# Kernel optimization log

Hardware: AMD Instinct MI355X
Metric: run time of the kernel (lower is better)

The kernel has to match this reference:

```python
import jax, jax.numpy as jnp
import numpy as np

HEAD = 12
EPS = float(np.finfo(np.float32).eps)  # torch RMSNorm default eps = finfo(dtype).eps


def _rmsnorm(v, g):
    # v: [B,H,T,dh], g: [dh]
    ms = jnp.mean(v * v, axis=-1, keepdims=True)
    return v * jax.lax.rsqrt(ms + EPS) * g


def setup_inputs() -> dict:
    key = jax.random.key(0)
    k1, k2, k3, k4, k5 = jax.random.split(key, 5)
    B, T, C = 2, 2048, 768
    x = jax.random.normal(k1, (B, T, C), dtype=jnp.float32)
    # nn.Linear(feats, feats, bias=False) weight: [out, in]
    W = jax.random.normal(k2, (C, C), dtype=jnp.float32) * (1.0 / np.sqrt(C))
    dh = C // HEAD
    g1 = jnp.ones((dh,), dtype=jnp.float32)
    g2 = jnp.ones((dh,), dtype=jnp.float32)
    g3 = jnp.ones((dh,), dtype=jnp.float32)
    return {"x": x, "W": W, "g1": g1, "g2": g2, "g3": g3}


def reference(x, W, g1, g2, g3):
    B, T, C = x.shape
    dh = C // HEAD
    sqrt_d = np.sqrt(dh).astype(np.float32)
    # qkv projection (shared weights): w = x @ W.T -> [B,H,T,dh]
    w = (x @ W.T).reshape(B, T, HEAD, dh).transpose(0, 2, 1, 3)
    q = _rmsnorm(w, g1)
    k = _rmsnorm(w, g2)
    v = _rmsnorm(w, g3)
    # full T x T score matrix (intentionally materialized, as in the module)
    att = jnp.einsum('bhif,bhjf->bhij', q, k) / sqrt_d
    a = jax.nn.softmax(att, axis=-1) + jax.nn.softmax(att, axis=-2)  # bisoftmax
    y = jnp.einsum('bhij,bhjf->bihf', a, v).reshape(B, T, C)
    # F.linear(y, W.t()) == y @ W
    return y @ W
```

## Files before the change

kernel.cpp:

```cpp
#include <hip/hip_runtime.h>

constexpr int T_SEQ = 2048;
constexpr int CDIM  = 768;
constexpr int HEADS = 12;
constexpr int DH    = 64;
constexpr int BATCH = 2;
constexpr int BH_TOT = BATCH * HEADS;
constexpr int NROWS  = BATCH * T_SEQ;
constexpr float RMS_EPS = 1.1920929e-07f;
constexpr float QSCALE = 0.18033688011112042f;

typedef __attribute__((ext_vector_type(8))) short bf16x8;
typedef __attribute__((ext_vector_type(4))) float f32x4;
typedef __attribute__((ext_vector_type(4))) unsigned int u32x4;

__device__ __forceinline__ unsigned short f2bf(float f) {
    union { float f; unsigned int u; } v; v.f = f;
    unsigned int u = v.u;
    unsigned int r = (u + 0x7fffu + ((u >> 16) & 1u)) >> 16;
    return (unsigned short)r;
}
__device__ __forceinline__ float b2f(unsigned short h) {
    union { unsigned int u; float f; } v; v.u = ((unsigned int)h) << 16;
    return v.f;
}
__device__ __forceinline__ unsigned int cvt_pk_bf16(float lo, float hi) {
    unsigned int r;
    asm("v_cvt_pk_bf16_f32 %0, %1, %2" : "=v"(r) : "v"(lo), "v"(hi));
    return r;
}
__device__ __forceinline__ float fast_exp2(float x) {
    float r;
    asm("v_exp_f32 %0, %1" : "=v"(r) : "v"(x));
    return r;
}
__device__ __forceinline__ void gld_lds16(const void* g, void* l) {
    __builtin_amdgcn_global_load_lds(
        (const __attribute__((address_space(1))) void*)g,
        (__attribute__((address_space(3))) void*)l, 16, 0, 0);
}
__device__ __forceinline__ void stage16k(const unsigned short* gbase, unsigned short* lbase, int tid) {
#pragma unroll
    for (int p = 0; p < 4; ++p) {
        int d = (p * 256 + tid) * 16;
        int gb = d ^ (((d >> 7) & 7) << 4);
        gld_lds16((const char*)gbase + gb, (char*)lbase + d);
    }
}
__device__ __forceinline__ void stageV16k(const unsigned short* vbase, int jbyte0,
                                          unsigned short* lbase, int tid) {
#pragma unroll
    for (int p = 0; p < 4; ++p) {
        int d = (p * 256 + tid) * 16;
        int f = d >> 8;
        int cb = (d & 255) ^ ((f & 7) << 4);
        gld_lds16((const char*)vbase + (size_t)f * (T_SEQ * 2) + jbyte0 + cb,
                  (char*)lbase + d);
    }
}

__global__ __launch_bounds__(256) void prep_kernel(
    const float* __restrict__ x, const float* __restrict__ W,
    unsigned short* __restrict__ xh,
    unsigned short* __restrict__ Wh, unsigned short* __restrict__ WTh)
{
    const size_t NC = (size_t)NROWS * CDIM;
    const size_t WSZ = (size_t)CDIM * CDIM;
    size_t stride = (size_t)gridDim.x * blockDim.x;
    for (size_t i = (size_t)blockIdx.x * blockDim.x + threadIdx.x; i < NC; i += stride)
        xh[i] = f2bf(x[i]);
    for (size_t i = (size_t)blockIdx.x * blockDim.x + threadIdx.x; i < WSZ; i += stride) {
        unsigned short h = f2bf(W[i]);
        Wh[i] = h;
        size_t k = i / CDIM, c = i % CDIM;
        WTh[c * CDIM + k] = h;
    }
}

__global__ __launch_bounds__(256) void gemm64_nt(
    const unsigned short* __restrict__ A, const unsigned short* __restrict__ B,
    float* __restrict__ C, int M, int N, int K, int ldc)
{
    __shared__ unsigned short sA[64 * 64], sB[64 * 64];
    const int tid = threadIdx.x;
    const int lane = tid & 63;
    const int wv = tid >> 6;
    const int wr = wv >> 1, wc = wv & 1;
    const int li = lane & 15, g = lane >> 4;
    const int M0 = blockIdx.y * 64, N0 = blockIdx.x * 64;

    f32x4 acc[2][2];
#pragma unroll
    for (int i = 0; i < 2; ++i)
#pragma unroll
        for (int j = 0; j < 2; ++j) acc[i][j] = (f32x4)0.0f;

    for (int k0 = 0; k0 < K; k0 += 64) {
        __syncthreads();
#pragma unroll
        for (int p = 0; p < 2; ++p) {
            int dd = tid * 16 + p * 4096;
            int row = dd >> 7;
            int cb = (dd & 127) ^ ((row & 7) << 4);
            gld_lds16((const char*)A + ((size_t)(M0 + row) * K + k0) * 2 + cb, (char*)sA + dd);
            gld_lds16((const char*)B + ((size_t)(N0 + row) * K + k0) * 2 + cb, (char*)sB + dd);
        }
        __syncthreads();
#pragma unroll
        for (int ks = 0; ks < 2; ++ks) {
            const int ko = ks * 32 + g * 8;
            bf16x8 a[2], b[2];
#pragma unroll
            for (int mi = 0; mi < 2; ++mi) {
                int r = wr * 32 + mi * 16 + li;
                a[mi] = *(const bf16x8*)((char*)sA + ((r * 128 + ko * 2) ^ ((r & 7) << 4)));
            }
#pragma unroll
            for (int ni = 0; ni < 2; ++ni) {
                int r = wc * 32 + ni * 16 + li;
                b[ni] = *(const bf16x8*)((char*)sB + ((r * 128 + ko * 2) ^ ((r & 7) << 4)));
            }
#pragma unroll
            for (int mi = 0; mi < 2; ++mi)
#pragma unroll
                for (int ni = 0; ni < 2; ++ni)
                    acc[mi][ni] = __builtin_amdgcn_mfma_f32_16x16x32_bf16(a[mi], b[ni], acc[mi][ni], 0, 0, 0);
        }
    }
#pragma unroll
    for (int mi = 0; mi < 2; ++mi)
#pragma unroll
        for (int ni = 0; ni < 2; ++ni)
#pragma unroll
            for (int r = 0; r < 4; ++r) {
                int row = M0 + wr * 32 + mi * 16 + g * 4 + r;
                int col = N0 + wc * 32 + ni * 16 + li;
                C[(size_t)row * ldc + col] = acc[mi][ni][r];
            }
}

__global__ __launch_bounds__(256) void rmsqkv_kernel(
    const float* __restrict__ wbuf,
    const float* __restrict__ g1, const float* __restrict__ g2, const float* __restrict__ g3,
    unsigned short* __restrict__ qb, unsigned short* __restrict__ kb,
    unsigned short* __restrict__ vb)
{
    const int lane = threadIdx.x & 63;
    const int wv = threadIdx.x >> 6;
    const int ridx = blockIdx.x * 4 + wv;
    const int bt = ridx / HEADS;
    const int h = ridx % HEADS;
    const int b = bt >> 11, t = bt & (T_SEQ - 1);

    float v = wbuf[(size_t)bt * CDIM + h * DH + lane];
    float ss = v * v;
#pragma unroll
    for (int m = 32; m; m >>= 1) ss += __shfl_xor(ss, m);
    float r = rsqrtf(ss * (1.0f / 64.0f) + RMS_EPS);
    float wn = v * r;

    size_t o = ((size_t)(b * HEADS + h) * T_SEQ + t) * DH + lane;
    qb[o] = f2bf(wn * g1[lane] * QSCALE);
    kb[o] = f2bf(wn * g2[lane]);
    vb[o] = f2bf(wn * g3[lane]);
}

__global__ __launch_bounds__(256) void vtrans_kernel(
    const unsigned short* __restrict__ vb, unsigned short* __restrict__ vT)
{
    __shared__ unsigned short tile[64][65];
    const int bh = blockIdx.y, t0 = blockIdx.x * 64;
    const int tid = threadIdx.x;
    const int c = tid & 63, r4 = tid >> 6;
#pragma unroll
    for (int i = 0; i < 16; ++i) {
        int rr = r4 + i * 4;
        tile[rr][c] = vb[((size_t)bh * T_SEQ + t0 + rr) * DH + c];
    }
    __syncthreads();
#pragma unroll
    for (int i = 0; i < 16; ++i) {
        int ff = r4 + i * 4;
        vT[((size_t)bh * DH + ff) * T_SEQ + t0 + c] = tile[c][ff];
    }
}

__global__ __launch_bounds__(256) void sums_kernel(
    const unsigned short* __restrict__ qb, const unsigned short* __restrict__ kb,
    float* __restrict__ rowsum, float* __restrict__ colsum)
{
    __shared__ unsigned short sQ[2][128 * 64];
    const int tid = threadIdx.x;
    const int lane = tid & 63;
    const int w = tid >> 6;
    const int li = lane & 15;
    const int g = lane >> 4;
    const int bh = blockIdx.z;
    const int J0 = blockIdx.x * 128;
    const int IC = blockIdx.y * 512;

    bf16x8 kf[2][2];
#pragma unroll
    for (int jb = 0; jb < 2; ++jb)
#pragma unroll
        for (int ks = 0; ks < 2; ++ks)
            kf[jb][ks] = *(const bf16x8*)&kb[((size_t)bh * T_SEQ + J0 + w * 32 + jb * 16 + li) * DH
                                            + ks * 32 + g * 8];

    stage16k(&qb[((size_t)bh * T_SEQ + IC) * DH], sQ[0], tid);
    __syncthreads();

    float csum[2][4];
#pragma unroll
    for (int jb = 0; jb < 2; ++jb)
#pragma unroll
        for (int r = 0; r < 4; ++r) csum[jb][r] = 0.0f;

    for (int it = 0; it < 4; ++it) {
        const int I0 = IC + it * 128;
        if (it + 1 < 4)
            stage16k(&qb[((size_t)bh * T_SEQ + I0 + 128) * DH], sQ[(it + 1) & 1], tid);
        const unsigned short* q = sQ[it & 1];

#pragma unroll
        for (int half = 0; half < 2; ++half) {
            f32x4 acc[2][4];
#pragma unroll
            for (int jb = 0; jb < 2; ++jb)
#pragma unroll
                for (int ib = 0; ib < 4; ++ib) acc[jb][ib] = (f32x4)0.0f;
#pragma unroll
            for (int ks = 0; ks < 2; ++ks) {
                const int ko = ks * 32 + g * 8;
#pragma unroll
                for (int ib = 0; ib < 4; ++ib) {
                    int qr = half * 64 + ib * 16 + li;
                    bf16x8 qf = *(const bf16x8*)((const char*)q + ((qr * 128 + ko * 2) ^ ((qr & 7) << 4)));
#pragma unroll
                    for (int jb = 0; jb < 2; ++jb)
                        acc[jb][ib] = __builtin_amdgcn_mfma_f32_16x16x32_bf16(kf[jb][ks], qf, acc[jb][ib], 0, 0, 0);
                }
            }
#pragma unroll
            for (int ib = 0; ib < 4; ++ib) {
                float rp = 0.0f;
#pragma unroll
                for (int jb = 0; jb < 2; ++jb)
#pragma unroll
                    for (int r = 0; r < 4; ++r) {
                        float e = fast_exp2(acc[jb][ib][r]);
                        csum[jb][r] += e;
                        rp += e;
                    }
                rp += __shfl_xor(rp, 16);
                rp += __shfl_xor(rp, 32);
                if (g == 0)
                    atomicAdd(&rowsum[(size_t)bh * T_SEQ + I0 + half * 64 + ib * 16 + li], rp);
            }
        }
        __syncthreads();
    }
#pragma unroll
    for (int jb = 0; jb < 2; ++jb)
#pragma unroll
        for (int r = 0; r < 4; ++r) {
            float c = csum[jb][r];
            c += __shfl_xor(c, 1); c += __shfl_xor(c, 2);
            c += __shfl_xor(c, 4); c += __shfl_xor(c, 8);
            if (li == 0)
                atomicAdd(&colsum[(size_t)bh * T_SEQ + J0 + w * 32 + jb * 16 + g * 4 + r], c);
        }
}

__global__ __launch_bounds__(256) void inv_kernel(
    const float* __restrict__ rs, const float* __restrict__ cs,
    float* __restrict__ ri, float* __restrict__ ci_, int n)
{
    int i = blockIdx.x * 256 + threadIdx.x;
    if (i < n) { ri[i] = 1.0f / rs[i]; ci_[i] = 1.0f / cs[i]; }
}

__global__ __launch_bounds__(256) void fused_pv_kernel(
    const unsigned short* __restrict__ qb, const unsigned short* __restrict__ kb,
    const unsigned short* __restrict__ vT,
    const float* __restrict__ rowinv, const float* __restrict__ colinv,
    float* __restrict__ ypart, int jlen, int nt)
{
    __shared__ unsigned short sK[2][128 * 64];
    __shared__ unsigned short sV[2][64 * 128];
    __shared__ unsigned short sP[64 * 128];

    const int tid = threadIdx.x;
    const int lane = tid & 63;
    const int w = tid >> 6;
    const int li = lane & 15;
    const int g = lane >> 4;
    const int bh = blockIdx.z;
    const int jc = blockIdx.y;
    const int I0 = blockIdx.x * 64;
    const int J0 = jc * jlen;

    const int qrow = I0 + w * 16 + li;
    bf16x8 qf[2];
#pragma unroll
    for (int ks = 0; ks < 2; ++ks)
        qf[ks] = *(const bf16x8*)&qb[((size_t)bh * T_SEQ + qrow) * DH + ks * 32 + g * 8];
    const float rv = rowinv[bh * T_SEQ + qrow];

    const int prow = w * 16 + li;
    const int pkey = (prow & 7) << 4;

    f32x4 accy[4];
#pragma unroll
    for (int i = 0; i < 4; ++i) accy[i] = (f32x4)0.0f;

    const unsigned short* kt0 = &kb[((size_t)bh * T_SEQ + J0) * DH];
    const unsigned short* vb0 = &vT[(size_t)bh * DH * T_SEQ];

    stage16k(kt0, sK[0], tid);
    stageV16k(vb0, J0 * 2, sV[0], tid);

    int buf = 0;
    for (int jt = 0; jt < nt; ++jt) {
        __syncthreads();
        if (jt + 1 < nt) {
            stage16k(kt0 + (size_t)(jt + 1) * 128 * DH, sK[buf ^ 1], tid);
            stageV16k(vb0, (J0 + (jt + 1) * 128) * 2, sV[buf ^ 1], tid);
        }

        f32x4 accs[8];
#pragma unroll
        for (int jb = 0; jb < 8; ++jb) accs[jb] = (f32x4)0.0f;
#pragma unroll
        for (int ks = 0; ks < 2; ++ks) {
            const int ko = ks * 32 + g * 8;
#pragma unroll
            for (int jb = 0; jb < 8; ++jb) {
                int jr = jb * 16 + li;
                bf16x8 kfr = *(const bf16x8*)((char*)sK[buf] + ((jr * 128 + ko * 2) ^ ((jr & 7) << 4)));
                accs[jb] = __builtin_amdgcn_mfma_f32_16x16x32_bf16(kfr, qf[ks], accs[jb], 0, 0, 0);
            }
        }

#pragma unroll
        for (int jb = 0; jb < 8; ++jb) {
            f32x4 cv = *(const f32x4*)&colinv[(size_t)bh * T_SEQ + J0 + jt * 128 + jb * 16 + g * 4];
            float p0 = fast_exp2(accs[jb][0]) * (rv + cv[0]);
            float p1 = fast_exp2(accs[jb][1]) * (rv + cv[1]);
            float p2 = fast_exp2(accs[jb][2]) * (rv + cv[2]);
            float p3 = fast_exp2(accs[jb][3]) * (rv + cv[3]);
            uint2 pw;
            pw.x = cvt_pk_bf16(p0, p1);
            pw.y = cvt_pk_bf16(p2, p3);
            int off = (prow * 256 + jb * 32 + g * 8) ^ pkey;
            *(uint2*)((char*)sP + off) = pw;
        }

#pragma unroll
        for (int ks2 = 0; ks2 < 4; ++ks2) {
            bf16x8 pf = *(const bf16x8*)((char*)sP + ((prow * 256 + ks2 * 64 + g * 16) ^ pkey));
#pragma unroll
            for (int ni = 0; ni < 4; ++ni) {
                int vrow = ni * 16 + li;
                bf16x8 vf = *(const bf16x8*)((char*)sV[buf] + ((vrow * 256 + ks2 * 64 + g * 16) ^ ((vrow & 7) << 4)));
                accy[ni] = __builtin_amdgcn_mfma_f32_16x16x32_bf16(pf, vf, accy[ni], 0, 0, 0);
            }
        }
        buf ^= 1;
    }

#pragma unroll
    for (int ni = 0; ni < 4; ++ni)
#pragma unroll
        for (int r = 0; r < 4; ++r) {
            int i = I0 + w * 16 + g * 4 + r;
            int f = ni * 16 + li;
            ypart[(((size_t)jc * BH_TOT + bh) * T_SEQ + i) * DH + f] = accy[ni][r];
        }
}

__global__ __launch_bounds__(256) void reduce_kernel(
    const float* __restrict__ ypart, unsigned short* __restrict__ yh, int js)
{
    const size_t STR = (size_t)BH_TOT * T_SEQ * DH;
    size_t idx = (size_t)blockIdx.x * 256 + threadIdx.x;
    if (idx >= STR / 4) return;
    f32x4 a = *(const f32x4*)&ypart[idx * 4];
    for (int c = 1; c < js; ++c) {
        f32x4 b = *(const f32x4*)&ypart[(size_t)c * STR + idx * 4];
        a[0] += b[0]; a[1] += b[1]; a[2] += b[2]; a[3] += b[3];
    }
    int e = (int)(idx * 4);
    int f = e & 63;
    int rrow = e >> 6;
    int t = rrow & (T_SEQ - 1);
    int bh = rrow >> 11;
    int b_ = bh / HEADS, h = bh % HEADS;
    size_t o = ((size_t)b_ * T_SEQ + t) * CDIM + h * DH + f;
#pragma unroll
    for (int q = 0; q < 4; ++q)
        yh[o + q] = f2bf(a[q]);
}

extern "C" void kernel_launch(void* const* d_in, const int* in_sizes, int n_in,
                              void* d_out, int out_size, void* d_ws, size_t ws_size,
                              hipStream_t stream)
{
    const float* x  = (const float*)d_in[0];
    const float* W  = (const float*)d_in[1];
    const float* g1 = (const float*)d_in[2];
    const float* g2 = (const float*)d_in[3];
    const float* g3 = (const float*)d_in[4];
    float* out = (float*)d_out;

    char* p = (char*)d_ws;
    auto alloc = [&](size_t bytes) -> void* {
        void* r = (void*)p;
        p += (bytes + 255) & ~(size_t)255;
        return r;
    };
    const size_t NC  = (size_t)NROWS * CDIM;
    const size_t WSZ = (size_t)CDIM * CDIM;
    const size_t QSZ = (size_t)BH_TOT * T_SEQ * DH;

    unsigned short* xh   = (unsigned short*)alloc(NC * 2);
    unsigned short* Wh   = (unsigned short*)alloc(WSZ * 2);
    unsigned short* WTh  = (unsigned short*)alloc(WSZ * 2);
    float*          wbuf = (float*)alloc(NC * 4);
    unsigned short* qb   = (unsigned short*)alloc(QSZ * 2);
    unsigned short* kb   = (unsigned short*)alloc(QSZ * 2);
    unsigned short* vb   = (unsigned short*)alloc(QSZ * 2);
    unsigned short* vT   = (unsigned short*)alloc(QSZ * 2);
    unsigned short* yh   = (unsigned short*)alloc(NC * 2);
    float* rowsum = (float*)alloc((size_t)BH_TOT * T_SEQ * 4);
    float* colsum = (float*)alloc((size_t)BH_TOT * T_SEQ * 4);
    float* rowinv = (float*)alloc((size_t)BH_TOT * T_SEQ * 4);
    float* colinv = (float*)alloc((size_t)BH_TOT * T_SEQ * 4);

    size_t used = (size_t)(p - (char*)d_ws);
    int js = (ws_size >= used + 4 * QSZ * sizeof(float) + (1u << 20)) ? 4 : 2;
    float* ypart = (float*)alloc((size_t)js * QSZ * 4);

    prep_kernel<<<2048, 256, 0, stream>>>(x, W, xh, Wh, WTh);
    gemm64_nt<<<dim3(CDIM / 64, NROWS / 64), 256, 0, stream>>>(
        xh, Wh, wbuf, NROWS, CDIM, CDIM, CDIM);
    rmsqkv_kernel<<<(NROWS * HEADS) / 4, 256, 0, stream>>>(
        wbuf, g1, g2, g3, qb, kb, vb);
    vtrans_kernel<<<dim3(T_SEQ / 64, BH_TOT), 256, 0, stream>>>(vb, vT);

    hipMemsetAsync(rowsum, 0, (size_t)BH_TOT * T_SEQ * 4, stream);
    hipMemsetAsync(colsum, 0, (size_t)BH_TOT * T_SEQ * 4, stream);
    sums_kernel<<<dim3(T_SEQ / 128, 4, BH_TOT), 256, 0, stream>>>(
        qb, kb, rowsum, colsum);
    int n = BH_TOT * T_SEQ;
    inv_kernel<<<(n + 255) / 256, 256, 0, stream>>>(rowsum, colsum, rowinv, colinv, n);

    fused_pv_kernel<<<dim3(T_SEQ / 64, js, BH_TOT), 256, 0, stream>>>(
        qb, kb, vT, rowinv, colinv, ypart, T_SEQ / js, T_SEQ / js / 128);
    {
        size_t n4 = (size_t)BH_TOT * T_SEQ * DH / 4;
        reduce_kernel<<<(unsigned)((n4 + 255) / 256), 256, 0, stream>>>(ypart, yh, js);
    }

    gemm64_nt<<<dim3(CDIM / 64, NROWS / 64), 256, 0, stream>>>(
        yh, WTh, out, NROWS, CDIM, CDIM, CDIM);
}
```

Baseline: 164.4 us.

## Pre-arrange LDS tiles in MFMA fragment order and fix split-J to two

Replaces the XOR-swizzled row-major LDS staging of Q, K, V and the P scratch with layouts stored directly in MFMA fragment order. Each lane's 16-byte fragment read becomes a simple linear offset, which removes swizzle arithmetic and is meant to avoid bank conflicts. The J-split is also hardcoded to two chunks, so the loop trip count is a compile-time constant and the reduce step is a fixed two-way add. The cost is less parallelism in the fused PV kernel than when four splits were chosen, and global loads during staging are now gathered in smaller strided pieces.

```diff
diff --git a/kernel.cpp b/kernel.cpp
--- a/kernel.cpp
+++ b/kernel.cpp
@@ -7,6 +7,7 @@
 constexpr int BATCH = 2;
 constexpr int BH_TOT = BATCH * HEADS;
 constexpr int NROWS  = BATCH * T_SEQ;
+constexpr int JS     = 2;
 constexpr float RMS_EPS = 1.1920929e-07f;
 constexpr float QSCALE = 0.18033688011112042f;
 
@@ -39,23 +40,34 @@
         (const __attribute__((address_space(1))) void*)g,
         (__attribute__((address_space(3))) void*)l, 16, 0, 0);
 }
-__device__ __forceinline__ void stage16k(const unsigned short* gbase, unsigned short* lbase, int tid) {
+__device__ __forceinline__ void stageK(const unsigned short* gbase, unsigned short* lbase, int tid) {
 #pragma unroll
     for (int p = 0; p < 4; ++p) {
-        int d = (p * 256 + tid) * 16;
-        int gb = d ^ (((d >> 7) & 7) << 4);
-        gld_lds16((const char*)gbase + gb, (char*)lbase + d);
-    }
-}
-__device__ __forceinline__ void stageV16k(const unsigned short* vbase, int jbyte0,
-                                          unsigned short* lbase, int tid) {
+        int d16 = p * 256 + tid;
+        int li = d16 & 15, g = (d16 >> 4) & 3, ks = (d16 >> 6) & 1, jb = d16 >> 7;
+        int src = (jb * 16 + li) * 128 + ks * 64 + g * 16;
+        gld_lds16((const char*)gbase + src, (char*)lbase + d16 * 16);
+    }
+}
+__device__ __forceinline__ void stageV(const unsigned short* vbase, int jbyte0,
+                                       unsigned short* lbase, int tid) {
 #pragma unroll
     for (int p = 0; p < 4; ++p) {
-        int d = (p * 256 + tid) * 16;
-        int f = d >> 8;
-        int cb = (d & 255) ^ ((f & 7) << 4);
-        gld_lds16((const char*)vbase + (size_t)f * (T_SEQ * 2) + jbyte0 + cb,
-                  (char*)lbase + d);
+        int d16 = p * 256 + tid;
+        int li = d16 & 15, g = (d16 >> 4) & 3, ni = (d16 >> 6) & 3, ks2 = d16 >> 8;
+        int f = ni * 16 + li;
+        gld_lds16((const char*)vbase + (size_t)f * (T_SEQ * 2) + jbyte0 + ks2 * 64 + g * 16,
+                  (char*)lbase + d16 * 16);
+    }
+}
+__device__ __forceinline__ void stageQ(const unsigned short* gbase, unsigned short* lbase, int tid) {
+#pragma unroll
+    for (int p = 0; p < 4; ++p) {
+        int d16 = p * 256 + tid;
+        int li = d16 & 15, g = (d16 >> 4) & 3, ks = (d16 >> 6) & 1;
+        int ib = (d16 >> 7) & 3, half = (d16 >> 9) & 1;
+        int src = (half * 64 + ib * 16 + li) * 128 + ks * 64 + g * 16;
+        gld_lds16((const char*)gbase + src, (char*)lbase + d16 * 16);
     }
 }
 
@@ -207,7 +219,7 @@
             kf[jb][ks] = *(const bf16x8*)&kb[((size_t)bh * T_SEQ + J0 + w * 32 + jb * 16 + li) * DH
                                             + ks * 32 + g * 8];
 
-    stage16k(&qb[((size_t)bh * T_SEQ + IC) * DH], sQ[0], tid);
+    stageQ(&qb[((size_t)bh * T_SEQ + IC) * DH], sQ[0], tid);
     __syncthreads();
 
     float csum[2][4];
@@ -219,7 +231,7 @@
     for (int it = 0; it < 4; ++it) {
         const int I0 = IC + it * 128;
         if (it + 1 < 4)
-            stage16k(&qb[((size_t)bh * T_SEQ + I0 + 128) * DH], sQ[(it + 1) & 1], tid);
+            stageQ(&qb[((size_t)bh * T_SEQ + I0 + 128) * DH], sQ[(it + 1) & 1], tid);
         const unsigned short* q = sQ[it & 1];
 
 #pragma unroll
@@ -231,11 +243,10 @@
                 for (int ib = 0; ib < 4; ++ib) acc[jb][ib] = (f32x4)0.0f;
 #pragma unroll
             for (int ks = 0; ks < 2; ++ks) {
-                const int ko = ks * 32 + g * 8;
 #pragma unroll
                 for (int ib = 0; ib < 4; ++ib) {
-                    int qr = half * 64 + ib * 16 + li;
-                    bf16x8 qf = *(const bf16x8*)((const char*)q + ((qr * 128 + ko * 2) ^ ((qr & 7) << 4)));
+                    bf16x8 qf = *(const bf16x8*)((const char*)q +
+                        ((((half * 4 + ib) * 2 + ks) * 64 + g * 16 + li) * 16));
 #pragma unroll
                     for (int jb = 0; jb < 2; ++jb)
                         acc[jb][ib] = __builtin_amdgcn_mfma_f32_16x16x32_bf16(kf[jb][ks], qf, acc[jb][ib], 0, 0, 0);
@@ -284,7 +295,7 @@
     const unsigned short* __restrict__ qb, const unsigned short* __restrict__ kb,
     const unsigned short* __restrict__ vT,
     const float* __restrict__ rowinv, const float* __restrict__ colinv,
-    float* __restrict__ ypart, int jlen, int nt)
+    float* __restrict__ ypart)
 {
     __shared__ unsigned short sK[2][128 * 64];
     __shared__ unsigned short sV[2][64 * 128];
@@ -298,7 +309,8 @@
     const int bh = blockIdx.z;
     const int jc = blockIdx.y;
     const int I0 = blockIdx.x * 64;
-    const int J0 = jc * jlen;
+    const int J0 = jc * (T_SEQ / JS);
+    constexpr int NT = T_SEQ / JS / 128;
 
     const int qrow = I0 + w * 16 + li;
     bf16x8 qf[2];
@@ -307,8 +319,7 @@
         qf[ks] = *(const bf16x8*)&qb[((size_t)bh * T_SEQ + qrow) * DH + ks * 32 + g * 8];
     const float rv = rowinv[bh * T_SEQ + qrow];
 
-    const int prow = w * 16 + li;
-    const int pkey = (prow & 7) << 4;
+    char* const sPw = (char*)sP + w * 4096;
 
     f32x4 accy[4];
 #pragma unroll
@@ -317,15 +328,15 @@
     const unsigned short* kt0 = &kb[((size_t)bh * T_SEQ + J0) * DH];
     const unsigned short* vb0 = &vT[(size_t)bh * DH * T_SEQ];
 
-    stage16k(kt0, sK[0], tid);
-    stageV16k(vb0, J0 * 2, sV[0], tid);
+    stageK(kt0, sK[0], tid);
+    stageV(vb0, J0 * 2, sV[0], tid);
 
     int buf = 0;
-    for (int jt = 0; jt < nt; ++jt) {
+    for (int jt = 0; jt < NT; ++jt) {
         __syncthreads();
-        if (jt + 1 < nt) {
-            stage16k(kt0 + (size_t)(jt + 1) * 128 * DH, sK[buf ^ 1], tid);
-            stageV16k(vb0, (J0 + (jt + 1) * 128) * 2, sV[buf ^ 1], tid);
+        if (jt + 1 < NT) {
+            stageK(kt0 + (size_t)(jt + 1) * 128 * DH, sK[buf ^ 1], tid);
+            stageV(vb0, (J0 + (jt + 1) * 128) * 2, sV[buf ^ 1], tid);
         }
 
         f32x4 accs[8];
@@ -333,11 +344,10 @@
         for (int jb = 0; jb < 8; ++jb) accs[jb] = (f32x4)0.0f;
 #pragma unroll
         for (int ks = 0; ks < 2; ++ks) {
-            const int ko = ks * 32 + g * 8;
 #pragma unroll
             for (int jb = 0; jb < 8; ++jb) {
-                int jr = jb * 16 + li;
-                bf16x8 kfr = *(const bf16x8*)((char*)sK[buf] + ((jr * 128 + ko * 2) ^ ((jr & 7) << 4)));
+                bf16x8 kfr = *(const bf16x8*)((char*)sK[buf] +
+                    (((jb * 2 + ks) * 64 + g * 16 + li) * 16));
                 accs[jb] = __builtin_amdgcn_mfma_f32_16x16x32_bf16(kfr, qf[ks], accs[jb], 0, 0, 0);
             }
         }
@@ -352,17 +362,17 @@
             uint2 pw;
             pw.x = cvt_pk_bf16(p0, p1);
             pw.y = cvt_pk_bf16(p2, p3);
-            int off = (prow * 256 + jb * 32 + g * 8) ^ pkey;
-            *(uint2*)((char*)sP + off) = pw;
+            int off = ((jb >> 1) * 4 + (jb & 1) * 2 + (g >> 1)) * 256 + li * 16 + (g & 1) * 8;
+            *(uint2*)(sPw + off) = pw;
         }
 
 #pragma unroll
         for (int ks2 = 0; ks2 < 4; ++ks2) {
-            bf16x8 pf = *(const bf16x8*)((char*)sP + ((prow * 256 + ks2 * 64 + g * 16) ^ pkey));
+            bf16x8 pf = *(const bf16x8*)(sPw + ((ks2 * 4 + g) * 256 + li * 16));
 #pragma unroll
             for (int ni = 0; ni < 4; ++ni) {
-                int vrow = ni * 16 + li;
-                bf16x8 vf = *(const bf16x8*)((char*)sV[buf] + ((vrow * 256 + ks2 * 64 + g * 16) ^ ((vrow & 7) << 4)));
+                bf16x8 vf = *(const bf16x8*)((char*)sV[buf] +
+                    ((ks2 * 256 + ni * 64 + g * 16 + li) * 16));
                 accy[ni] = __builtin_amdgcn_mfma_f32_16x16x32_bf16(pf, vf, accy[ni], 0, 0, 0);
             }
         }
@@ -380,16 +390,13 @@
 }
 
 __global__ __launch_bounds__(256) void reduce_kernel(
-    const float* __restrict__ ypart, unsigned short* __restrict__ yh, int js)
+    const float* __restrict__ ypart, unsigned short* __restrict__ yh)
 {
     const size_t STR = (size_t)BH_TOT * T_SEQ * DH;
     size_t idx = (size_t)blockIdx.x * 256 + threadIdx.x;
     if (idx >= STR / 4) return;
     f32x4 a = *(const f32x4*)&ypart[idx * 4];
-    for (int c = 1; c < js; ++c) {
-        f32x4 b = *(const f32x4*)&ypart[(size_t)c * STR + idx * 4];
-        a[0] += b[0]; a[1] += b[1]; a[2] += b[2]; a[3] += b[3];
-    }
+    f32x4 b = *(const f32x4*)&ypart[STR + idx * 4];
     int e = (int)(idx * 4);
     int f = e & 63;
     int rrow = e >> 6;
@@ -399,7 +406,7 @@
     size_t o = ((size_t)b_ * T_SEQ + t) * CDIM + h * DH + f;
 #pragma unroll
     for (int q = 0; q < 4; ++q)
-        yh[o + q] = f2bf(a[q]);
+        yh[o + q] = f2bf(a[q] + b[q]);
 }
 
 extern "C" void kernel_launch(void* const* d_in, const int* in_sizes, int n_in,
@@ -432,14 +439,11 @@
     unsigned short* vb   = (unsigned short*)alloc(QSZ * 2);
     unsigned short* vT   = (unsigned short*)alloc(QSZ * 2);
     unsigned short* yh   = (unsigned short*)alloc(NC * 2);
+    float* ypart  = (float*)alloc((size_t)JS * QSZ * 4);
     float* rowsum = (float*)alloc((size_t)BH_TOT * T_SEQ * 4);
     float* colsum = (float*)alloc((size_t)BH_TOT * T_SEQ * 4);
     float* rowinv = (float*)alloc((size_t)BH_TOT * T_SEQ * 4);
     float* colinv = (float*)alloc((size_t)BH_TOT * T_SEQ * 4);
-
-    size_t used = (size_t)(p - (char*)d_ws);
-    int js = (ws_size >= used + 4 * QSZ * sizeof(float) + (1u << 20)) ? 4 : 2;
-    float* ypart = (float*)alloc((size_t)js * QSZ * 4);
 
     prep_kernel<<<2048, 256, 0, stream>>>(x, W, xh, Wh, WTh);
     gemm64_nt<<<dim3(CDIM / 64, NROWS / 64), 256, 0, stream>>>(
@@ -455,11 +459,11 @@
     int n = BH_TOT * T_SEQ;
     inv_kernel<<<(n + 255) / 256, 256, 0, stream>>>(rowsum, colsum, rowinv, colinv, n);
 
-    fused_pv_kernel<<<dim3(T_SEQ / 64, js, BH_TOT), 256, 0, stream>>>(
-        qb, kb, vT, rowinv, colinv, ypart, T_SEQ / js, T_SEQ / js / 128);
+    fused_pv_kernel<<<dim3(T_SEQ / 64, JS, BH_TOT), 256, 0, stream>>>(
+        qb, kb, vT, rowinv, colinv, ypart);
     {
         size_t n4 = (size_t)BH_TOT * T_SEQ * DH / 4;
-        reduce_kernel<<<(unsigned)((n4 + 255) / 256), 256, 0, stream>>>(ypart, yh, js);
+        reduce_kernel<<<(unsigned)((n4 + 255) / 256), 256, 0, stream>>>(ypart, yh);
     }
 
     gemm64_nt<<<dim3(CDIM / 64, NROWS / 64), 256, 0, stream>>>(
```

After: 165.6 us. No clear change (+0.7%).
